# Performance work log

Hardware: AMD Instinct MI355X
Metric: run time of the kernel (lower is better)

The kernel has to match this reference:

```python
import jax, jax.numpy as jnp
import numpy as np

N_NODES = 50000
N_EDGES = 600000
N_GRAPHS = 1000
IN_DIM = 128   # atom_feat_dim
HID = 128      # emb_dim
NEG_SLOPE = 0.01


def setup_inputs() -> dict:
    key = jax.random.key(0)
    k = jax.random.split(key, 6)
    drug_x = jax.random.normal(k[0], (N_NODES, IN_DIM), dtype=jnp.float32)
    edge_index = jax.random.randint(k[1], (2, N_EDGES), 0, N_NODES, dtype=jnp.int32)
    batch = jnp.sort(jax.random.randint(k[2], (N_NODES,), 0, N_GRAPHS, dtype=jnp.int32))
    # GCNConv parameters (glorot-ish init for weights, zero bias, as in PyG)
    W1 = jax.random.normal(k[3], (IN_DIM, HID), dtype=jnp.float32) * (1.0 / np.sqrt(IN_DIM))
    b1 = jnp.zeros((HID,), dtype=jnp.float32)
    W2 = jax.random.normal(k[4], (HID, HID), dtype=jnp.float32) * (1.0 / np.sqrt(HID))
    b2 = jnp.zeros((HID,), dtype=jnp.float32)
    return {"drug_x": drug_x, "W1": W1, "b1": b1, "W2": W2, "b2": b2,
            "edge_index": edge_index, "batch": batch}


def _gcn_conv(x, W, b, src, dst, n_nodes):
    """PyG GCNConv: lin -> add self-loops -> deg^-1/2 sym norm -> scatter-add -> +bias."""
    h = x @ W  # [N, H]
    ones = jnp.ones(src.shape[0], dtype=h.dtype)
    # degree on the target side, +1 for the self-loop
    deg = jax.ops.segment_sum(ones, dst, num_segments=n_nodes) + 1.0
    dinv = jax.lax.rsqrt(deg)  # [N]
    coef = dinv[src] * dinv[dst]  # [E]
    agg = jax.ops.segment_sum(h[src] * coef[:, None], dst, num_segments=n_nodes)
    # self-loop contribution: dinv[i]*dinv[i]*h[i]
    agg = agg + h * (dinv * dinv)[:, None]
    return agg + b


def _leaky_relu(x):
    return jnp.where(x > 0, x, NEG_SLOPE * x)


def reference(drug_x, W1, b1, W2, b2, edge_index, batch):
    src, dst = edge_index[0], edge_index[1]
    n = drug_x.shape[0]
    h = _leaky_relu(_gcn_conv(drug_x, W1, b1, src, dst, n))  # dropout = identity (eval)
    h = _leaky_relu(_gcn_conv(h, W2, b2, src, dst, n))
    # global_mean_pool over graph ids
    sums = jax.ops.segment_sum(h, batch, num_segments=N_GRAPHS)
    counts = jax.ops.segment_sum(jnp.ones((n,), h.dtype), batch, num_segments=N_GRAPHS)
    return sums / jnp.maximum(counts, 1.0)[:, None]
```

## Files before the change

### kernel.cpp

```cpp
#include <hip/hip_runtime.h>

#define DIM 128
#define NEG_SLOPE 0.01f
#define ELLW 64
#define CPAD 16
#define LDA 136

typedef short short8 __attribute__((ext_vector_type(8)));
typedef float f32x4 __attribute__((ext_vector_type(4)));

__device__ __forceinline__ unsigned short f2bf(float f) {
    unsigned u = __float_as_uint(f);
    u = u + 0x7FFFu + ((u >> 16) & 1u);
    return (unsigned short)(u >> 16);
}
__device__ __forceinline__ float bf2f(unsigned short s) {
    return __uint_as_float((unsigned)s << 16);
}

__global__ __launch_bounds__(256) void k_fillprep(const int* __restrict__ src,
                                                  const int* __restrict__ dst,
                                                  int* __restrict__ cursorPad,
                                                  int* __restrict__ eSrc,
                                                  const float* __restrict__ W1,
                                                  const float* __restrict__ W2,
                                                  unsigned short* __restrict__ Wt1,
                                                  unsigned short* __restrict__ Wt2,
                                                  int nE) {
    int i = blockIdx.x * 256 + threadIdx.x;
    if (i < nE) {
        int s = src[i], d = dst[i];
        int pos = atomicAdd(&cursorPad[d * CPAD], 1);
        if (pos < ELLW) eSrc[(size_t)d * ELLW + pos] = s;
    }
    if (i < 32768) {
        const float* W = (i < 16384) ? W1 : W2;
        unsigned short* Wt = (i < 16384) ? Wt1 : Wt2;
        int j = i & 16383;
        int k = j >> 7, n = j & 127;
        Wt[n * 128 + k] = f2bf(W[k * 128 + n]);
    }
}

__global__ __launch_bounds__(256) void k_gemm(const float* __restrict__ X,
                                              const unsigned short* __restrict__ Wt,
                                              const int* __restrict__ cursorPad,
                                              unsigned short* __restrict__ Y, int nRows) {
    __shared__ unsigned short sA[64 * LDA];
    const int t = threadIdx.x;
    const int row0 = blockIdx.x * 64;

#pragma unroll
    for (int rep = 0; rep < 8; ++rep) {
        int idx = t + rep * 256;
        int r = idx >> 5, k4 = (idx & 31) * 4;
        int gr = row0 + r;
        float4 v = make_float4(0.f, 0.f, 0.f, 0.f);
        if (gr < nRows) v = *(const float4*)&X[(size_t)gr * 128 + k4];
        ushort4 p;
        p.x = f2bf(v.x); p.y = f2bf(v.y); p.z = f2bf(v.z); p.w = f2bf(v.w);
        *(ushort4*)&sA[r * LDA + k4] = p;
    }
    __syncthreads();

    const int wave = t >> 6, lane = t & 63;
    const int l15 = lane & 15;
    const int koff = (lane >> 4) * 8;
    const int arow = wave * 16 + l15;

    short8 a[4];
#pragma unroll
    for (int ks = 0; ks < 4; ++ks)
        a[ks] = *(const short8*)&sA[arow * LDA + ks * 32 + koff];

    f32x4 acc[8];
#pragma unroll
    for (int c = 0; c < 8; ++c) acc[c] = (f32x4){0.f, 0.f, 0.f, 0.f};
#pragma unroll
    for (int c = 0; c < 8; ++c) {
        const unsigned short* wp = Wt + (size_t)(c * 16 + l15) * 128 + koff;
#pragma unroll
        for (int ks = 0; ks < 4; ++ks) {
            short8 b = *(const short8*)(wp + ks * 32);
            acc[c] = __builtin_amdgcn_mfma_f32_16x16x32_bf16(a[ks], b, acc[c], 0, 0, 0);
        }
    }
    const int orow = row0 + wave * 16 + (lane >> 4) * 4;
#pragma unroll
    for (int r = 0; r < 4; ++r) {
        int gr = orow + r;
        if (gr < nRows) {
            float dv = rsqrtf((float)cursorPad[gr * CPAD] + 1.0f);
#pragma unroll
            for (int c = 0; c < 8; ++c)
                Y[(size_t)gr * 128 + c * 16 + l15] = f2bf(acc[c][r] * dv);
        }
    }
}

__global__ __launch_bounds__(256) void k_gemm_bf(const unsigned short* __restrict__ Xb,
                                                 const unsigned short* __restrict__ Wt,
                                                 const int* __restrict__ cursorPad,
                                                 unsigned short* __restrict__ Y, int nRows) {
    __shared__ unsigned short sA[64 * LDA];
    const int t = threadIdx.x;
    const int row0 = blockIdx.x * 64;

#pragma unroll
    for (int rep = 0; rep < 4; ++rep) {
        int idx = t + rep * 256;
        int r = idx >> 4, c8 = (idx & 15) * 8;
        int gr = row0 + r;
        uint4 v = make_uint4(0, 0, 0, 0);
        if (gr < nRows) v = *(const uint4*)&Xb[(size_t)gr * 128 + c8];
        *(uint4*)&sA[r * LDA + c8] = v;
    }
    __syncthreads();

    const int wave = t >> 6, lane = t & 63;
    const int l15 = lane & 15;
    const int koff = (lane >> 4) * 8;
    const int arow = wave * 16 + l15;

    short8 a[4];
#pragma unroll
    for (int ks = 0; ks < 4; ++ks)
        a[ks] = *(const short8*)&sA[arow * LDA + ks * 32 + koff];

    f32x4 acc[8];
#pragma unroll
    for (int c = 0; c < 8; ++c) acc[c] = (f32x4){0.f, 0.f, 0.f, 0.f};
#pragma unroll
    for (int c = 0; c < 8; ++c) {
        const unsigned short* wp = Wt + (size_t)(c * 16 + l15) * 128 + koff;
#pragma unroll
        for (int ks = 0; ks < 4; ++ks) {
            short8 b = *(const short8*)(wp + ks * 32);
            acc[c] = __builtin_amdgcn_mfma_f32_16x16x32_bf16(a[ks], b, acc[c], 0, 0, 0);
        }
    }
    const int orow = row0 + wave * 16 + (lane >> 4) * 4;
#pragma unroll
    for (int r = 0; r < 4; ++r) {
        int gr = orow + r;
        if (gr < nRows) {
            float dv = rsqrtf((float)cursorPad[gr * CPAD] + 1.0f);
#pragma unroll
            for (int c = 0; c < 8; ++c)
                Y[(size_t)gr * 128 + c * 16 + l15] = f2bf(acc[c][r] * dv);
        }
    }
}

#define ACCUM(v)                                         \
    do {                                                 \
        acc[0] += bf2f((v).x & 0xFFFFu);                 \
        acc[1] += __uint_as_float((v).x & 0xFFFF0000u);  \
        acc[2] += bf2f((v).y & 0xFFFFu);                 \
        acc[3] += __uint_as_float((v).y & 0xFFFF0000u);  \
        acc[4] += bf2f((v).z & 0xFFFFu);                 \
        acc[5] += __uint_as_float((v).z & 0xFFFF0000u);  \
        acc[6] += bf2f((v).w & 0xFFFFu);                 \
        acc[7] += __uint_as_float((v).w & 0xFFFF0000u);  \
    } while (0)

__global__ __launch_bounds__(256) void k_gather_bf(const uint4* __restrict__ h4,
                                                   const int* __restrict__ cursorPad,
                                                   const int* __restrict__ eSrc,
                                                   const float* __restrict__ bias,
                                                   unsigned short* __restrict__ outH,
                                                   int n) {
    const int g = threadIdx.x >> 4;
    const int l = threadIdx.x & 15;
    const int i = blockIdx.x * 16 + g;
    if (i >= n) return;
    const int beg = i * ELLW;
    const int cnt = cursorPad[i * CPAD];
    const int deg = min(cnt, ELLW);
    const int end = beg + deg;
    const float di = rsqrtf((float)cnt + 1.0f);

    float acc[8];
    {
        uint4 hv = h4[(size_t)i * 16 + l];
        acc[0] = bf2f(hv.x & 0xFFFFu);
        acc[1] = __uint_as_float(hv.x & 0xFFFF0000u);
        acc[2] = bf2f(hv.y & 0xFFFFu);
        acc[3] = __uint_as_float(hv.y & 0xFFFF0000u);
        acc[4] = bf2f(hv.z & 0xFFFFu);
        acc[5] = __uint_as_float(hv.z & 0xFFFF0000u);
        acc[6] = bf2f(hv.w & 0xFFFFu);
        acc[7] = __uint_as_float(hv.w & 0xFFFF0000u);
    }
    int e = beg;
    for (; e + 8 <= end; e += 8) {
        int4 s0 = *(const int4*)&eSrc[e];
        int4 s1 = *(const int4*)&eSrc[e + 4];
        uint4 v[8];
        v[0] = h4[(size_t)s0.x * 16 + l];
        v[1] = h4[(size_t)s0.y * 16 + l];
        v[2] = h4[(size_t)s0.z * 16 + l];
        v[3] = h4[(size_t)s0.w * 16 + l];
        v[4] = h4[(size_t)s1.x * 16 + l];
        v[5] = h4[(size_t)s1.y * 16 + l];
        v[6] = h4[(size_t)s1.z * 16 + l];
        v[7] = h4[(size_t)s1.w * 16 + l];
#pragma unroll
        for (int j = 0; j < 8; ++j) ACCUM(v[j]);
    }
    if (e + 4 <= end) {
        int4 s0 = *(const int4*)&eSrc[e];
        uint4 v[4];
        v[0] = h4[(size_t)s0.x * 16 + l];
        v[1] = h4[(size_t)s0.y * 16 + l];
        v[2] = h4[(size_t)s0.z * 16 + l];
        v[3] = h4[(size_t)s0.w * 16 + l];
#pragma unroll
        for (int j = 0; j < 4; ++j) ACCUM(v[j]);
        e += 4;
    }
    if (e + 2 <= end) {
        int s0 = eSrc[e], s1 = eSrc[e + 1];
        uint4 v0 = h4[(size_t)s0 * 16 + l];
        uint4 v1 = h4[(size_t)s1 * 16 + l];
        ACCUM(v0);
        ACCUM(v1);
        e += 2;
    }
    if (e < end) {
        int s0 = eSrc[e];
        uint4 v0 = h4[(size_t)s0 * 16 + l];
        ACCUM(v0);
    }

    float4 b0 = *(const float4*)&bias[l * 8];
    float4 b1 = *(const float4*)&bias[l * 8 + 4];
    acc[0] = acc[0] * di + b0.x; acc[0] = acc[0] > 0.f ? acc[0] : NEG_SLOPE * acc[0];
    acc[1] = acc[1] * di + b0.y; acc[1] = acc[1] > 0.f ? acc[1] : NEG_SLOPE * acc[1];
    acc[2] = acc[2] * di + b0.z; acc[2] = acc[2] > 0.f ? acc[2] : NEG_SLOPE * acc[2];
    acc[3] = acc[3] * di + b0.w; acc[3] = acc[3] > 0.f ? acc[3] : NEG_SLOPE * acc[3];
    acc[4] = acc[4] * di + b1.x; acc[4] = acc[4] > 0.f ? acc[4] : NEG_SLOPE * acc[4];
    acc[5] = acc[5] * di + b1.y; acc[5] = acc[5] > 0.f ? acc[5] : NEG_SLOPE * acc[5];
    acc[6] = acc[6] * di + b1.z; acc[6] = acc[6] > 0.f ? acc[6] : NEG_SLOPE * acc[6];
    acc[7] = acc[7] * di + b1.w; acc[7] = acc[7] > 0.f ? acc[7] : NEG_SLOPE * acc[7];

    ushort4 p0, p1;
    p0.x = f2bf(acc[0]); p0.y = f2bf(acc[1]); p0.z = f2bf(acc[2]); p0.w = f2bf(acc[3]);
    p1.x = f2bf(acc[4]); p1.y = f2bf(acc[5]); p1.z = f2bf(acc[6]); p1.w = f2bf(acc[7]);
    *(ushort4*)&outH[(size_t)i * 128 + l * 8] = p0;
    *(ushort4*)&outH[(size_t)i * 128 + l * 8 + 4] = p1;
}
#undef ACCUM

__global__ __launch_bounds__(128) void k_pool(const unsigned short* __restrict__ h,
                                              const int* __restrict__ batch,
                                              float* __restrict__ out, int nG, int nN) {
    int g = blockIdx.x;
    int c = threadIdx.x;
    int lo = 0, hi = nN;
    while (lo < hi) { int m = (lo + hi) >> 1; if (batch[m] < g) lo = m + 1; else hi = m; }
    int beg = lo;
    hi = nN;
    while (lo < hi) { int m = (lo + hi) >> 1; if (batch[m] < g + 1) lo = m + 1; else hi = m; }
    int end = lo;
    float acc = 0.0f;
    for (int r = beg; r < end; ++r) acc += bf2f(h[(size_t)r * DIM + c]);
    out[(size_t)g * DIM + c] = acc / fmaxf((float)(end - beg), 1.0f);
}

extern "C" void kernel_launch(void* const* d_in, const int* in_sizes, int n_in,
                              void* d_out, int out_size, void* d_ws, size_t ws_size,
                              hipStream_t stream) {
    const float* X  = (const float*)d_in[0];
    const float* W1 = (const float*)d_in[1];
    const float* b1 = (const float*)d_in[2];
    const float* W2 = (const float*)d_in[3];
    const float* b2 = (const float*)d_in[4];
    const int*   ei = (const int*)d_in[5];
    const int*   batch = (const int*)d_in[6];
    float* out = (float*)d_out;

    const int NN = in_sizes[0] / DIM;
    const int NE = in_sizes[5] / 2;
    const int NG = out_size / DIM;

    const int* src = ei;
    const int* dst = ei + NE;

    char* ws = (char*)d_ws;
    size_t o = 0;
    auto alloc = [&](size_t bytes) {
        char* p = ws + o;
        o += (bytes + 1023) & ~(size_t)1023;
        return p;
    };
    int* cursorPad = (int*)alloc((size_t)NN * CPAD * 4);
    unsigned short* Wt1 = (unsigned short*)alloc((size_t)16384 * 2);
    unsigned short* Wt2 = (unsigned short*)alloc((size_t)16384 * 2);
    int*   eSrc    = (int*)alloc((size_t)NN * ELLW * 4);
    unsigned short* bufHa = (unsigned short*)alloc((size_t)NN * DIM * 2);
    unsigned short* bufHb = (unsigned short*)alloc((size_t)NN * DIM * 2);

    hipMemsetAsync(cursorPad, 0, (size_t)NN * CPAD * 4, stream);

    const int B = 256;

    k_fillprep<<<(NE + B - 1) / B, B, 0, stream>>>(src, dst, cursorPad, eSrc,
                                                   W1, W2, Wt1, Wt2, NE);

    int gemm_grid = (NN + 63) / 64;
    int gather_grid = (NN + 15) / 16;

    k_gemm<<<gemm_grid, B, 0, stream>>>(X, Wt1, cursorPad, bufHa, NN);
    k_gather_bf<<<gather_grid, B, 0, stream>>>((const uint4*)bufHa, cursorPad, eSrc,
                                               b1, bufHb, NN);

    k_gemm_bf<<<gemm_grid, B, 0, stream>>>(bufHb, Wt2, cursorPad, bufHa, NN);
    k_gather_bf<<<gather_grid, B, 0, stream>>>((const uint4*)bufHa, cursorPad, eSrc,
                                               b2, bufHb, NN);

    k_pool<<<NG, 128, 0, stream>>>(bufHb, batch, out, NG, NN);
}
```

Baseline: 228.6 us.

## Fuse gather into second GEMM and second gather into mean pooling

Fuses the layer-1 aggregation with the layer-2 GEMM: each 64-row tile gathers neighbours into shared memory and then runs the MFMA GEMM, so the intermediate activation is never written to or re-read from global memory. It also fuses the layer-2 aggregation with global mean pooling, with one block per graph accumulating into shared memory through atomics, which removes the final activation buffer and the separate pool kernel. In exchange, k_gp parallelism is limited to 1000 blocks of about 50 nodes each, and shared-memory atomics on 128 slots contend across 16 node groups. The k_gg gather runs four sequential passes per thread before the GEMM.

```diff
diff --git a/kernel.cpp b/kernel.cpp
--- a/kernel.cpp
+++ b/kernel.cpp
@@ -98,60 +98,6 @@
     }
 }
 
-__global__ __launch_bounds__(256) void k_gemm_bf(const unsigned short* __restrict__ Xb,
-                                                 const unsigned short* __restrict__ Wt,
-                                                 const int* __restrict__ cursorPad,
-                                                 unsigned short* __restrict__ Y, int nRows) {
-    __shared__ unsigned short sA[64 * LDA];
-    const int t = threadIdx.x;
-    const int row0 = blockIdx.x * 64;
-
-#pragma unroll
-    for (int rep = 0; rep < 4; ++rep) {
-        int idx = t + rep * 256;
-        int r = idx >> 4, c8 = (idx & 15) * 8;
-        int gr = row0 + r;
-        uint4 v = make_uint4(0, 0, 0, 0);
-        if (gr < nRows) v = *(const uint4*)&Xb[(size_t)gr * 128 + c8];
-        *(uint4*)&sA[r * LDA + c8] = v;
-    }
-    __syncthreads();
-
-    const int wave = t >> 6, lane = t & 63;
-    const int l15 = lane & 15;
-    const int koff = (lane >> 4) * 8;
-    const int arow = wave * 16 + l15;
-
-    short8 a[4];
-#pragma unroll
-    for (int ks = 0; ks < 4; ++ks)
-        a[ks] = *(const short8*)&sA[arow * LDA + ks * 32 + koff];
-
-    f32x4 acc[8];
-#pragma unroll
-    for (int c = 0; c < 8; ++c) acc[c] = (f32x4){0.f, 0.f, 0.f, 0.f};
-#pragma unroll
-    for (int c = 0; c < 8; ++c) {
-        const unsigned short* wp = Wt + (size_t)(c * 16 + l15) * 128 + koff;
-#pragma unroll
-        for (int ks = 0; ks < 4; ++ks) {
-            short8 b = *(const short8*)(wp + ks * 32);
-            acc[c] = __builtin_amdgcn_mfma_f32_16x16x32_bf16(a[ks], b, acc[c], 0, 0, 0);
-        }
-    }
-    const int orow = row0 + wave * 16 + (lane >> 4) * 4;
-#pragma unroll
-    for (int r = 0; r < 4; ++r) {
-        int gr = orow + r;
-        if (gr < nRows) {
-            float dv = rsqrtf((float)cursorPad[gr * CPAD] + 1.0f);
-#pragma unroll
-            for (int c = 0; c < 8; ++c)
-                Y[(size_t)gr * 128 + c * 16 + l15] = f2bf(acc[c][r] * dv);
-        }
-    }
-}
-
 #define ACCUM(v)                                         \
     do {                                                 \
         acc[0] += bf2f((v).x & 0xFFFFu);                 \
@@ -164,23 +110,17 @@
         acc[7] += __uint_as_float((v).w & 0xFFFF0000u);  \
     } while (0)
 
-__global__ __launch_bounds__(256) void k_gather_bf(const uint4* __restrict__ h4,
-                                                   const int* __restrict__ cursorPad,
-                                                   const int* __restrict__ eSrc,
-                                                   const float* __restrict__ bias,
-                                                   unsigned short* __restrict__ outH,
-                                                   int n) {
-    const int g = threadIdx.x >> 4;
-    const int l = threadIdx.x & 15;
-    const int i = blockIdx.x * 16 + g;
-    if (i >= n) return;
+__device__ __forceinline__ void gather_body(const uint4* __restrict__ h4,
+                                            const int* __restrict__ cursorPad,
+                                            const int* __restrict__ eSrc,
+                                            const float* __restrict__ bias,
+                                            int i, int l, float* acc) {
     const int beg = i * ELLW;
     const int cnt = cursorPad[i * CPAD];
     const int deg = min(cnt, ELLW);
     const int end = beg + deg;
     const float di = rsqrtf((float)cnt + 1.0f);
 
-    float acc[8];
     {
         uint4 hv = h4[(size_t)i * 16 + l];
         acc[0] = bf2f(hv.x & 0xFFFFu);
@@ -243,29 +183,112 @@
     acc[5] = acc[5] * di + b1.y; acc[5] = acc[5] > 0.f ? acc[5] : NEG_SLOPE * acc[5];
     acc[6] = acc[6] * di + b1.z; acc[6] = acc[6] > 0.f ? acc[6] : NEG_SLOPE * acc[6];
     acc[7] = acc[7] * di + b1.w; acc[7] = acc[7] > 0.f ? acc[7] : NEG_SLOPE * acc[7];
-
-    ushort4 p0, p1;
-    p0.x = f2bf(acc[0]); p0.y = f2bf(acc[1]); p0.z = f2bf(acc[2]); p0.w = f2bf(acc[3]);
-    p1.x = f2bf(acc[4]); p1.y = f2bf(acc[5]); p1.z = f2bf(acc[6]); p1.w = f2bf(acc[7]);
-    *(ushort4*)&outH[(size_t)i * 128 + l * 8] = p0;
-    *(ushort4*)&outH[(size_t)i * 128 + l * 8 + 4] = p1;
 }
 #undef ACCUM
 
-__global__ __launch_bounds__(128) void k_pool(const unsigned short* __restrict__ h,
-                                              const int* __restrict__ batch,
-                                              float* __restrict__ out, int nG, int nN) {
-    int g = blockIdx.x;
-    int c = threadIdx.x;
-    int lo = 0, hi = nN;
-    while (lo < hi) { int m = (lo + hi) >> 1; if (batch[m] < g) lo = m + 1; else hi = m; }
-    int beg = lo;
-    hi = nN;
-    while (lo < hi) { int m = (lo + hi) >> 1; if (batch[m] < g + 1) lo = m + 1; else hi = m; }
-    int end = lo;
-    float acc = 0.0f;
-    for (int r = beg; r < end; ++r) acc += bf2f(h[(size_t)r * DIM + c]);
-    out[(size_t)g * DIM + c] = acc / fmaxf((float)(end - beg), 1.0f);
+__global__ __launch_bounds__(256) void k_gg(const uint4* __restrict__ h4in,
+                                            const int* __restrict__ cursorPad,
+                                            const int* __restrict__ eSrc,
+                                            const float* __restrict__ bias,
+                                            const unsigned short* __restrict__ Wt,
+                                            unsigned short* __restrict__ Y, int nN) {
+    __shared__ unsigned short sA[64 * LDA];
+    const int t = threadIdx.x;
+    const int row0 = blockIdx.x * 64;
+    const int lg = t >> 4;
+    const int l = t & 15;
+
+#pragma unroll
+    for (int p = 0; p < 4; ++p) {
+        int r = p * 16 + lg;
+        int i = row0 + r;
+        float acc[8];
+        if (i < nN) {
+            gather_body(h4in, cursorPad, eSrc, bias, i, l, acc);
+        } else {
+#pragma unroll
+            for (int j = 0; j < 8; ++j) acc[j] = 0.0f;
+        }
+        ushort4 p0, p1;
+        p0.x = f2bf(acc[0]); p0.y = f2bf(acc[1]); p0.z = f2bf(acc[2]); p0.w = f2bf(acc[3]);
+        p1.x = f2bf(acc[4]); p1.y = f2bf(acc[5]); p1.z = f2bf(acc[6]); p1.w = f2bf(acc[7]);
+        *(ushort4*)&sA[r * LDA + l * 8] = p0;
+        *(ushort4*)&sA[r * LDA + l * 8 + 4] = p1;
+    }
+    __syncthreads();
+
+    const int wave = t >> 6, lane = t & 63;
+    const int l15 = lane & 15;
+    const int koff = (lane >> 4) * 8;
+    const int arow = wave * 16 + l15;
+
+    short8 a[4];
+#pragma unroll
+    for (int ks = 0; ks < 4; ++ks)
+        a[ks] = *(const short8*)&sA[arow * LDA + ks * 32 + koff];
+
+    f32x4 acc[8];
+#pragma unroll
+    for (int c = 0; c < 8; ++c) acc[c] = (f32x4){0.f, 0.f, 0.f, 0.f};
+#pragma unroll
+    for (int c = 0; c < 8; ++c) {
+        const unsigned short* wp = Wt + (size_t)(c * 16 + l15) * 128 + koff;
+#pragma unroll
+        for (int ks = 0; ks < 4; ++ks) {
+            short8 b = *(const short8*)(wp + ks * 32);
+            acc[c] = __builtin_amdgcn_mfma_f32_16x16x32_bf16(a[ks], b, acc[c], 0, 0, 0);
+        }
+    }
+    const int orow = row0 + wave * 16 + (lane >> 4) * 4;
+#pragma unroll
+    for (int r = 0; r < 4; ++r) {
+        int gr = orow + r;
+        if (gr < nN) {
+            float dv = rsqrtf((float)cursorPad[gr * CPAD] + 1.0f);
+#pragma unroll
+            for (int c = 0; c < 8; ++c)
+                Y[(size_t)gr * 128 + c * 16 + l15] = f2bf(acc[c][r] * dv);
+        }
+    }
+}
+
+__global__ __launch_bounds__(256) void k_gp(const uint4* __restrict__ h4in,
+                                            const int* __restrict__ cursorPad,
+                                            const int* __restrict__ eSrc,
+                                            const float* __restrict__ bias,
+                                            const int* __restrict__ batch,
+                                            float* __restrict__ out, int nN, int nG) {
+    __shared__ float accS[128];
+    __shared__ int bounds[2];
+    const int g = blockIdx.x;
+    const int t = threadIdx.x;
+    if (t < 128) accS[t] = 0.0f;
+    if (t == 0) {
+        int lo = 0, hi = nN;
+        while (lo < hi) { int m = (lo + hi) >> 1; if (batch[m] < g) lo = m + 1; else hi = m; }
+        bounds[0] = lo;
+        hi = nN;
+        while (lo < hi) { int m = (lo + hi) >> 1; if (batch[m] < g + 1) lo = m + 1; else hi = m; }
+        bounds[1] = lo;
+    }
+    __syncthreads();
+    const int beg = bounds[0], end = bounds[1];
+    const int lg = t >> 4, l = t & 15;
+
+    for (int base = beg; base < end; base += 16) {
+        int i = base + lg;
+        if (i < end) {
+            float acc[8];
+            gather_body(h4in, cursorPad, eSrc, bias, i, l, acc);
+#pragma unroll
+            for (int j = 0; j < 8; ++j) atomicAdd(&accS[l * 8 + j], acc[j]);
+        }
+    }
+    __syncthreads();
+    if (t < 128) {
+        float cnt = (float)(end - beg);
+        out[(size_t)g * DIM + t] = accS[t] / fmaxf(cnt, 1.0f);
+    }
 }
 
 extern "C" void kernel_launch(void* const* d_in, const int* in_sizes, int n_in,
@@ -298,8 +321,8 @@
     unsigned short* Wt1 = (unsigned short*)alloc((size_t)16384 * 2);
     unsigned short* Wt2 = (unsigned short*)alloc((size_t)16384 * 2);
     int*   eSrc    = (int*)alloc((size_t)NN * ELLW * 4);
-    unsigned short* bufHa = (unsigned short*)alloc((size_t)NN * DIM * 2);
-    unsigned short* bufHb = (unsigned short*)alloc((size_t)NN * DIM * 2);
+    unsigned short* bufA = (unsigned short*)alloc((size_t)NN * DIM * 2);
+    unsigned short* bufB = (unsigned short*)alloc((size_t)NN * DIM * 2);
 
     hipMemsetAsync(cursorPad, 0, (size_t)NN * CPAD * 4, stream);
 
@@ -308,16 +331,13 @@
     k_fillprep<<<(NE + B - 1) / B, B, 0, stream>>>(src, dst, cursorPad, eSrc,
                                                    W1, W2, Wt1, Wt2, NE);
 
-    int gemm_grid = (NN + 63) / 64;
-    int gather_grid = (NN + 15) / 16;
-
-    k_gemm<<<gemm_grid, B, 0, stream>>>(X, Wt1, cursorPad, bufHa, NN);
-    k_gather_bf<<<gather_grid, B, 0, stream>>>((const uint4*)bufHa, cursorPad, eSrc,
-                                               b1, bufHb, NN);
-
-    k_gemm_bf<<<gemm_grid, B, 0, stream>>>(bufHb, Wt2, cursorPad, bufHa, NN);
-    k_gather_bf<<<gather_grid, B, 0, stream>>>((const uint4*)bufHa, cursorPad, eSrc,
-                                               b2, bufHb, NN);
-
-    k_pool<<<NG, 128, 0, stream>>>(bufHb, batch, out, NG, NN);
-}
+    int tile_grid = (NN + 63) / 64;
+
+    k_gemm<<<tile_grid, B, 0, stream>>>(X, Wt1, cursorPad, bufA, NN);
+
+    k_gg<<<tile_grid, B, 0, stream>>>((const uint4*)bufA, cursorPad, eSrc, b1,
+                                      Wt2, bufB, NN);
+
+    k_gp<<<NG, B, 0, stream>>>((const uint4*)bufB, cursorPad, eSrc, b2,
+                               batch, out, NN, NG);
+}
```

New measurement: 225.2 us. Within noise of the previous version (-1.5%).
